# Kernel optimization log

Hardware: AMD Instinct MI355X
Metric: run time of the kernel (lower is better)

Reference implementation:

```python
import jax, jax.numpy as jnp
import numpy as np

L, H = 3, 2048  # stacked LSTM cells, uniform width


def setup_inputs() -> dict:
    key = jax.random.key(0)
    ks = jax.random.split(key, 7)
    s = 1.0 / np.sqrt(H)  # torch default LSTM init scale
    x = jax.random.normal(ks[0], (H,), jnp.float32)
    W_ih = jax.random.normal(ks[1], (L, 4 * H, H), jnp.float32) * s
    W_hh = jax.random.normal(ks[2], (L, 4 * H, H), jnp.float32) * s
    b_ih = jax.random.normal(ks[3], (L, 4 * H), jnp.float32) * s
    b_hh = jax.random.normal(ks[4], (L, 4 * H), jnp.float32) * s
    h0 = jax.random.uniform(ks[5], (L, H), jnp.float32)  # th.rand init
    c0 = jax.random.uniform(ks[6], (L, H), jnp.float32)
    return {"x": x, "W_ih": W_ih, "W_hh": W_hh, "b_ih": b_ih, "b_hh": b_hh, "h0": h0, "c0": c0}


def reference(x, W_ih, W_hh, b_ih, b_hh, h0, c0):
    # Single-step (seq_len=1, batch=1) LSTM cell applied through L stacked layers;
    # output h of layer l is the input x of layer l+1. Gate order: i, f, g, o.
    def step(xcar, layer):
        Wi, Wh, bi, bh, h, c = layer
        gates = Wi @ xcar + Wh @ h + bi + bh          # [4H]
        i_, f_, g_, o_ = jnp.split(gates, 4)
        i_ = jax.nn.sigmoid(i_)
        f_ = jax.nn.sigmoid(f_)
        g_ = jnp.tanh(g_)
        o_ = jax.nn.sigmoid(o_)
        c_new = f_ * c + i_ * g_
        h_new = o_ * jnp.tanh(c_new)
        return h_new, None

    out, _ = jax.lax.scan(step, x, (W_ih, W_hh, b_ih, b_hh, h0, c0))
    return out.reshape(1, 1, -1)  # torch LSTM returns [seq=1, batch=1, H]
```

## Files before the change

kernel.cpp:

```cpp
#include <hip/hip_runtime.h>
#include <math.h>

#define H 2048
#define R (4 * H)
#define L 3
#define NROWS_P1 (R + L * R)

typedef float f4 __attribute__((ext_vector_type(4)));


__device__ __forceinline__ float wave_row_dot(const float* __restrict__ row,
                                              const float* __restrict__ vec,
                                              int lane) {
    const f4* r4 = (const f4*)row;
    const f4* v4 = (const f4*)vec;
    float acc0 = 0.f, acc1 = 0.f;
#pragma unroll
    for (int it = 0; it < (H / 4) / 128; ++it) {
        const int i0 = (2 * it) * 64 + lane;
        const int i1 = (2 * it + 1) * 64 + lane;
        f4 a0 = __builtin_nontemporal_load(r4 + i0);
        f4 a1 = __builtin_nontemporal_load(r4 + i1);
        f4 v0 = v4[i0];
        f4 v1 = v4[i1];
        acc0 = fmaf(a0.x, v0.x, acc0);
        acc1 = fmaf(a1.x, v1.x, acc1);
        acc0 = fmaf(a0.y, v0.y, acc0);
        acc1 = fmaf(a1.y, v1.y, acc1);
        acc0 = fmaf(a0.z, v0.z, acc0);
        acc1 = fmaf(a1.z, v1.z, acc1);
        acc0 = fmaf(a0.w, v0.w, acc0);
        acc1 = fmaf(a1.w, v1.w, acc1);
    }
    float acc = acc0 + acc1;
#pragma unroll
    for (int off = 32; off > 0; off >>= 1)
        acc += __shfl_down(acc, off);
    return acc;
}

__global__ __launch_bounds__(256) void phase1_kernel(
    const float* __restrict__ Wi0,
    const float* __restrict__ Wh,
    const float* __restrict__ bi,
    const float* __restrict__ bh,
    const float* __restrict__ x,
    const float* __restrict__ h0,
    float* __restrict__ xpart,
    float* __restrict__ pre)
{
    const int wid  = threadIdx.x >> 6;
    const int lane = threadIdx.x & 63;
    const int g = blockIdx.x * 4 + wid;

    const float* row;
    const float* vec;
    if (g < R) {
        row = Wi0 + (size_t)g * H;
        vec = x;
    } else {
        const int r = g - R;
        row = Wh + (size_t)r * H;
        vec = h0 + (r >> 13) * H;
    }

    const float tot = wave_row_dot(row, vec, lane);

    if (lane == 0) {
        if (g < R) {
            xpart[g] = tot;
        } else {
            const int r = g - R;
            pre[r] = tot + bi[r] + bh[r];
        }
    }
}

__global__ __launch_bounds__(256) void wix_kernel(
    const float* __restrict__ Wi,
    const float* __restrict__ x,
    float* __restrict__ xpart)
{
    const int wid  = threadIdx.x >> 6;
    const int lane = threadIdx.x & 63;
    const int g = blockIdx.x * 4 + wid;
    const float tot = wave_row_dot(Wi + (size_t)g * H, x, lane);
    if (lane == 0) xpart[g] = tot;
}

__global__ __launch_bounds__(256) void update_kernel(
    const float* __restrict__ pre_l,
    const float* __restrict__ xpart,
    const float* __restrict__ c0_l,
    float* __restrict__ h_out)
{
    const int j = blockIdx.x * blockDim.x + threadIdx.x;
    if (j >= H) return;

    const float gi = pre_l[j]         + xpart[j];
    const float gf = pre_l[H + j]     + xpart[H + j];
    const float gg = pre_l[2 * H + j] + xpart[2 * H + j];
    const float go = pre_l[3 * H + j] + xpart[3 * H + j];

    const float i_ = 1.f / (1.f + expf(-gi));
    const float f_ = 1.f / (1.f + expf(-gf));
    const float g_ = tanhf(gg);
    const float o_ = 1.f / (1.f + expf(-go));

    const float c_new = f_ * c0_l[j] + i_ * g_;
    h_out[j] = o_ * tanhf(c_new);
}

extern "C" void kernel_launch(void* const* d_in, const int* in_sizes, int n_in,
                              void* d_out, int out_size, void* d_ws, size_t ws_size,
                              hipStream_t stream) {
    const float* x    = (const float*)d_in[0];
    const float* W_ih = (const float*)d_in[1];
    const float* W_hh = (const float*)d_in[2];
    const float* b_ih = (const float*)d_in[3];
    const float* b_hh = (const float*)d_in[4];
    const float* h0   = (const float*)d_in[5];
    const float* c0   = (const float*)d_in[6];
    float* out = (float*)d_out;

    float* xpart = (float*)d_ws;
    float* pre   = xpart + R;
    float* xbuf1 = pre + L * R;
    float* xbuf2 = xbuf1 + H;

    const size_t Wstride = (size_t)R * H;

    phase1_kernel<<<NROWS_P1 / 4, 256, 0, stream>>>(
        W_ih, W_hh, b_ih, b_hh, x, h0, xpart, pre);

    update_kernel<<<H / 256, 256, 0, stream>>>(pre, xpart, c0, xbuf1);

    wix_kernel<<<R / 4, 256, 0, stream>>>(W_ih + Wstride, xbuf1, xpart);
    update_kernel<<<H / 256, 256, 0, stream>>>(pre + R, xpart, c0 + H, xbuf2);

    wix_kernel<<<R / 4, 256, 0, stream>>>(W_ih + 2 * Wstride, xbuf2, xpart);
    update_kernel<<<H / 256, 256, 0, stream>>>(pre + 2 * R, xpart, c0 + 2 * H, out);
}
```

Baseline: 374.9 us.

## Fuse all LSTM layer stages into one persistent kernel with grid barriers

Replaces the six separate kernel launches with a single persistent kernel of 1024 blocks. Each wave processes several matrix rows per phase, and the phases are separated by atomic-counter grid barriers. This is meant to remove launch overhead and the inter-kernel gaps between the small update kernels. It relies on all 1024 blocks being co-resident, which 256 CUs at 4 blocks each should allow. It adds barrier spin costs and a small init kernel launch.

```diff
diff --git a/kernel.cpp b/kernel.cpp
--- a/kernel.cpp
+++ b/kernel.cpp
@@ -4,10 +4,30 @@
 #define H 2048
 #define R (4 * H)
 #define L 3
-#define NROWS_P1 (R + L * R)
+#define NBLK 1024
+#define NWAVE (NBLK * 4)
+#define ROWS_P1 (R + L * R)
+#define RPW_P1 (ROWS_P1 / NWAVE)
+#define RPW_WIX (R / NWAVE)
+#define NBAR 8
 
 typedef float f4 __attribute__((ext_vector_type(4)));
 
+__device__ __forceinline__ void grid_barrier(unsigned* __restrict__ bar, int i) {
+    __syncthreads();
+    if (threadIdx.x == 0) {
+        __threadfence();
+        atomicAdd(&bar[i], 1u);
+        while (atomicAdd(&bar[i], 0u) < (unsigned)NBLK)
+            __builtin_amdgcn_s_sleep(8);
+    }
+    __syncthreads();
+    __threadfence();
+}
+
+__global__ void init_barriers(unsigned* __restrict__ bar) {
+    if (threadIdx.x < NBAR) bar[threadIdx.x] = 0u;
+}
 
 __device__ __forceinline__ float wave_row_dot(const float* __restrict__ row,
                                               const float* __restrict__ vec,
@@ -39,64 +59,11 @@
     return acc;
 }
 
-__global__ __launch_bounds__(256) void phase1_kernel(
-    const float* __restrict__ Wi0,
-    const float* __restrict__ Wh,
-    const float* __restrict__ bi,
-    const float* __restrict__ bh,
-    const float* __restrict__ x,
-    const float* __restrict__ h0,
-    float* __restrict__ xpart,
-    float* __restrict__ pre)
-{
-    const int wid  = threadIdx.x >> 6;
-    const int lane = threadIdx.x & 63;
-    const int g = blockIdx.x * 4 + wid;
-
-    const float* row;
-    const float* vec;
-    if (g < R) {
-        row = Wi0 + (size_t)g * H;
-        vec = x;
-    } else {
-        const int r = g - R;
-        row = Wh + (size_t)r * H;
-        vec = h0 + (r >> 13) * H;
-    }
-
-    const float tot = wave_row_dot(row, vec, lane);
-
-    if (lane == 0) {
-        if (g < R) {
-            xpart[g] = tot;
-        } else {
-            const int r = g - R;
-            pre[r] = tot + bi[r] + bh[r];
-        }
-    }
-}
-
-__global__ __launch_bounds__(256) void wix_kernel(
-    const float* __restrict__ Wi,
-    const float* __restrict__ x,
-    float* __restrict__ xpart)
-{
-    const int wid  = threadIdx.x >> 6;
-    const int lane = threadIdx.x & 63;
-    const int g = blockIdx.x * 4 + wid;
-    const float tot = wave_row_dot(Wi + (size_t)g * H, x, lane);
-    if (lane == 0) xpart[g] = tot;
-}
-
-__global__ __launch_bounds__(256) void update_kernel(
-    const float* __restrict__ pre_l,
-    const float* __restrict__ xpart,
-    const float* __restrict__ c0_l,
-    float* __restrict__ h_out)
-{
-    const int j = blockIdx.x * blockDim.x + threadIdx.x;
-    if (j >= H) return;
-
+__device__ __forceinline__ void lstm_update_elem(const float* __restrict__ pre_l,
+                                                 const float* __restrict__ xpart,
+                                                 const float* __restrict__ c0_l,
+                                                 float* __restrict__ h_out,
+                                                 int j) {
     const float gi = pre_l[j]         + xpart[j];
     const float gf = pre_l[H + j]     + xpart[H + j];
     const float gg = pre_l[2 * H + j] + xpart[2 * H + j];
@@ -109,6 +76,76 @@
 
     const float c_new = f_ * c0_l[j] + i_ * g_;
     h_out[j] = o_ * tanhf(c_new);
+}
+
+__global__ __launch_bounds__(256) void fused_lstm_kernel(
+    const float* __restrict__ Wi,
+    const float* __restrict__ Wh,
+    const float* __restrict__ bi,
+    const float* __restrict__ bh,
+    const float* __restrict__ x,
+    const float* __restrict__ h0,
+    const float* __restrict__ c0,
+    float* __restrict__ xpart,
+    float* __restrict__ pre,
+    float* __restrict__ xbuf1,
+    float* __restrict__ xbuf2,
+    unsigned* __restrict__ bar,
+    float* __restrict__ out)
+{
+    const int wid  = threadIdx.x >> 6;
+    const int lane = threadIdx.x & 63;
+    const int w    = blockIdx.x * 4 + wid;
+    const int tid  = blockIdx.x * 256 + threadIdx.x;
+
+#pragma unroll
+    for (int k = 0; k < RPW_P1; ++k) {
+        const int g = w * RPW_P1 + k;
+        const float* row;
+        const float* vec;
+        if (g < R) {
+            row = Wi + (size_t)g * H;
+            vec = x;
+        } else {
+            const int r = g - R;
+            row = Wh + (size_t)r * H;
+            vec = h0 + (r >> 13) * H;
+        }
+        const float tot = wave_row_dot(row, vec, lane);
+        if (lane == 0) {
+            if (g < R) {
+                xpart[g] = tot;
+            } else {
+                const int r = g - R;
+                pre[r] = tot + bi[r] + bh[r];
+            }
+        }
+    }
+    grid_barrier(bar, 0);
+
+    if (tid < H) lstm_update_elem(pre, xpart, c0, xbuf1, tid);
+    grid_barrier(bar, 1);
+
+#pragma unroll
+    for (int k = 0; k < RPW_WIX; ++k) {
+        const int g = w * RPW_WIX + k;
+        const float tot = wave_row_dot(Wi + (size_t)R * H + (size_t)g * H, xbuf1, lane);
+        if (lane == 0) xpart[g] = tot;
+    }
+    grid_barrier(bar, 2);
+
+    if (tid < H) lstm_update_elem(pre + R, xpart, c0 + H, xbuf2, tid);
+    grid_barrier(bar, 3);
+
+#pragma unroll
+    for (int k = 0; k < RPW_WIX; ++k) {
+        const int g = w * RPW_WIX + k;
+        const float tot = wave_row_dot(Wi + 2 * (size_t)R * H + (size_t)g * H, xbuf2, lane);
+        if (lane == 0) xpart[g] = tot;
+    }
+    grid_barrier(bar, 4);
+
+    if (tid < H) lstm_update_elem(pre + 2 * R, xpart, c0 + 2 * H, out, tid);
 }
 
 extern "C" void kernel_launch(void* const* d_in, const int* in_sizes, int n_in,
@@ -127,17 +164,11 @@
     float* pre   = xpart + R;
     float* xbuf1 = pre + L * R;
     float* xbuf2 = xbuf1 + H;
+    unsigned* bar = (unsigned*)(xbuf2 + H);
 
-    const size_t Wstride = (size_t)R * H;
+    init_barriers<<<1, 64, 0, stream>>>(bar);
 
-    phase1_kernel<<<NROWS_P1 / 4, 256, 0, stream>>>(
-        W_ih, W_hh, b_ih, b_hh, x, h0, xpart, pre);
-
-    update_kernel<<<H / 256, 256, 0, stream>>>(pre, xpart, c0, xbuf1);
-
-    wix_kernel<<<R / 4, 256, 0, stream>>>(W_ih + Wstride, xbuf1, xpart);
-    update_kernel<<<H / 256, 256, 0, stream>>>(pre + R, xpart, c0 + H, xbuf2);
-
-    wix_kernel<<<R / 4, 256, 0, stream>>>(W_ih + 2 * Wstride, xbuf2, xpart);
-    update_kernel<<<H / 256, 256, 0, stream>>>(pre + 2 * R, xpart, c0 + 2 * H, out);
+    fused_lstm_kernel<<<NBLK, 256, 0, stream>>>(
+        W_ih, W_hh, b_ih, b_hh, x, h0, c0,
+        xpart, pre, xbuf1, xbuf2, bar, out);
 }
```

Result: slower. 1.151 ms (+206.9%).
